# Optimization experiments

Hardware: AMD Instinct MI355X
Metric: run time of the kernel (lower is better)

## Reference

```python
import jax, jax.numpy as jnp
import numpy as np

ANISO = (0.096, 0.096, 0.096)
BIG = 1e10  # stands in for +inf feature distance
SMOOTH = 1e-05


def _minplus(f, axis, w):
    # exact 1D squared distance transform along `axis` via min-plus conv:
    # g[i] = min_j f[j] + (w*(i-j))^2 ; vectorized over all other dims.
    f = jnp.moveaxis(f, axis, -1)
    n = f.shape[-1]
    idx = jnp.arange(n, dtype=f.dtype)
    d2 = (w * (idx[:, None] - idx[None, :])) ** 2  # [j, i]
    g = jnp.min(f[..., :, None] + d2, axis=-2)
    return jnp.moveaxis(g, -1, axis)


def _edt_multilabel(labels, num_labels):
    # labels: [b, X, Y, Z] int, values in [1, num_labels]
    # Multi-label euclidean distance transform (edt.edt semantics on gt+1):
    # for each voxel, distance to nearest voxel carrying a DIFFERENT label,
    # scaled by ANISO. Computed as per-label squared EDT fields (separable
    # min-plus per axis, exact) combined by excluding the voxel's own label.
    fields = []
    for L in range(1, num_labels + 1):  # small fixed loop over classes
        f = jnp.where(labels == L, 0.0, BIG).astype(jnp.float32)
        for ax, w in zip((1, 2, 3), ANISO):
            f = _minplus(f, ax, w)
        fields.append(f)
    D = jnp.stack(fields, axis=0)  # [L, b, X, Y, Z] squared distances
    own = jnp.moveaxis(jax.nn.one_hot(labels - 1, num_labels, dtype=jnp.float32), -1, 0)
    d2 = jnp.min(jnp.where(own > 0, BIG, D), axis=0)  # nearest different label
    return jnp.sqrt(d2)


def setup_inputs() -> dict:
    key = jax.random.key(0)
    kx, ky = jax.random.split(key)
    x = jax.random.uniform(kx, (2, 3, 64, 64, 64), dtype=jnp.float32)  # softmax probs
    y = jax.random.randint(ky, (2, 1, 64, 64, 64), 0, 3)  # label map, classes 0..2
    return {"x": x, "y": y}


def reference(x, y):
    b, c = x.shape[:2]
    yi = y[:, 0]  # [b, X, Y, Z]
    # scatter_(1, gt, 1) -> one hot over channel dim
    y_onehot = jnp.moveaxis(jax.nn.one_hot(yi, c, dtype=x.dtype), -1, 1)  # [b,c,X,Y,Z]
    # dt = edt(gt + 1) + 1 ; all labels >=1 so every voxel is 'foreground'
    dt = (_edt_multilabel(yi + 1, c) + 1.0)[:, None]  # [b,1,X,Y,Z]
    fp = x * (1.0 - y_onehot) * dt
    fn = (1.0 - x) * y_onehot * dt
    # do_bg=False (non-batch-dice path): drop background channel
    fp = fp[:, 1:]
    fn = fn[:, 1:]
    return jnp.mean(fp) + jnp.mean(fn) + SMOOTH
```

## Files before the change

kernel.cpp:

```cpp
#include <hip/hip_runtime.h>
#include <math.h>

#define BIGV 10000000000.0f
#define WA   0.096f

__device__ __forceinline__ float seed_dist2(unsigned long long mask, int i) {
    const unsigned long long mr = mask >> i;
    const unsigned long long ml = mask << (63 - i);
    const int dr = mr ? __builtin_ctzll(mr) : 1000;
    const int dl = ml ? __builtin_clzll(ml) : 1000;
    const int d  = dr < dl ? dr : dl;
    const float t = WA * (float)d;
    return (d > 63) ? BIGV : t * t;
}

__global__ __launch_bounds__(256) void pass_xz_kernel(const int* __restrict__ lab,
                                                      float* __restrict__ D) {
    const int ys = blockIdx.x, b = blockIdx.y, zq = blockIdx.z;
    const int lane = threadIdx.x & 63;
    const int wv   = threadIdx.x >> 6;

    __shared__ float sm[3][64][64];

    const int* lp = lab + b * 262144 + ys * 64;
    for (int z = wv * 16, e = z + 16; z < e; ++z) {
        const int lv = lp[z * 4096 + lane];
        const unsigned long long mk0 = __ballot(lv == 0);
        const unsigned long long mk1 = __ballot(lv == 1);
        const unsigned long long mk2 = __ballot(lv == 2);
        sm[0][z][lane] = seed_dist2(mk0, lane);
        sm[1][z][lane] = seed_dist2(mk1, lane);
        sm[2][z][lane] = seed_dist2(mk2, lane);
    }
    __syncthreads();

    const int i0 = zq * 16 + wv * 4;
    float m0[4], m1[4], m2[4];
#pragma unroll
    for (int ii = 0; ii < 4; ++ii) m0[ii] = m1[ii] = m2[ii] = __builtin_inff();

    for (int j = 0; j < 64; ++j) {
        const float a0 = sm[0][j][lane];
        const float a1 = sm[1][j][lane];
        const float a2 = sm[2][j][lane];
        const float fb = (float)(i0 - j);
#pragma unroll
        for (int ii = 0; ii < 4; ++ii) {
            const float t = WA * (fb + (float)ii);
            m0[ii] = fminf(m0[ii], __builtin_fmaf(t, t, a0));
            m1[ii] = fminf(m1[ii], __builtin_fmaf(t, t, a1));
            m2[ii] = fminf(m2[ii], __builtin_fmaf(t, t, a2));
        }
    }

    float* Dp = D + b * 3 * 262144 + ys * 64;
#pragma unroll
    for (int ii = 0; ii < 4; ++ii) {
        const int zo = (i0 + ii) * 4096 + lane;
        Dp[zo]              = m0[ii];
        Dp[262144 + zo]     = m1[ii];
        Dp[2 * 262144 + zo] = m2[ii];
    }
}

__global__ __launch_bounds__(256) void pass_y_kernel(const float* __restrict__ x,
                                                     const int* __restrict__ lab,
                                                     const float* __restrict__ D,
                                                     float* __restrict__ out) {
    const int z = blockIdx.x, b = blockIdx.y, yq = blockIdx.z;
    const int lane = threadIdx.x & 63;
    const int wv   = threadIdx.x >> 6;

    __shared__ float sm[3][64][64];
    {
        const float4* Dp4 = (const float4*)(D + b * 3 * 262144 + z * 4096);
        float4* s4 = (float4*)&sm[0][0][0];
        for (int t = threadIdx.x; t < 1024; t += 256) {
            s4[t]        = Dp4[t];
            s4[1024 + t] = Dp4[65536 + t];
            s4[2048 + t] = Dp4[131072 + t];
        }
    }
    __syncthreads();

    const int i0 = yq * 16 + wv * 4;
    float m0[4], m1[4], m2[4];
#pragma unroll
    for (int ii = 0; ii < 4; ++ii) m0[ii] = m1[ii] = m2[ii] = __builtin_inff();

    for (int j = 0; j < 64; ++j) {
        const float a0 = sm[0][j][lane];
        const float a1 = sm[1][j][lane];
        const float a2 = sm[2][j][lane];
        const float fb = (float)(i0 - j);
#pragma unroll
        for (int ii = 0; ii < 4; ++ii) {
            const float t = WA * (fb + (float)ii);
            m0[ii] = fminf(m0[ii], __builtin_fmaf(t, t, a0));
            m1[ii] = fminf(m1[ii], __builtin_fmaf(t, t, a1));
            m2[ii] = fminf(m2[ii], __builtin_fmaf(t, t, a2));
        }
    }

    float part = 0.0f;
#pragma unroll
    for (int ii = 0; ii < 4; ++ii) {
        const int yy  = i0 + ii;
        const int off = z * 4096 + yy * 64 + lane;
        const int lv  = lab[b * 262144 + off];
        const float x1 = x[(b * 3 + 1) * 262144 + off];
        const float x2 = x[(b * 3 + 2) * 262144 + off];
        const float d0  = (lv == 0) ? BIGV : m0[ii];
        const float d1  = (lv == 1) ? BIGV : m1[ii];
        const float d2m = (lv == 2) ? BIGV : m2[ii];
        const float dt  = sqrtf(fminf(d0, fminf(d1, d2m))) + 1.0f;
        const float t1  = (lv == 1) ? (1.0f - x1) : x1;
        const float t2  = (lv == 2) ? (1.0f - x2) : x2;
        part += (t1 + t2) * dt;
    }

#pragma unroll
    for (int o = 32; o; o >>= 1) part += __shfl_down(part, o);
    if (lane == 0)
        atomicAdd(out, part * (1.0f / 1048576.0f));
    if (blockIdx.x == 0 && blockIdx.y == 0 && blockIdx.z == 0 && threadIdx.x == 0)
        atomicAdd(out, 1e-5f);
}

extern "C" void kernel_launch(void* const* d_in, const int* in_sizes, int n_in,
                              void* d_out, int out_size, void* d_ws, size_t ws_size,
                              hipStream_t stream) {
    const float* x = (const float*)d_in[0];
    const int*   y = (const int*)d_in[1];
    float* D   = (float*)d_ws;
    float* out = (float*)d_out;

    hipMemsetAsync(out, 0, sizeof(float), stream);
    pass_xz_kernel<<<dim3(64, 2, 4), 256, 0, stream>>>(y, D);
    pass_y_kernel<<<dim3(64, 2, 4), 256, 0, stream>>>(x, y, D, out);
}
```

Before: 103.0 us.

## Fuse both EDT passes into one cooperative kernel with grid sync

Merges the xz-pass and y-pass kernels into a single cooperative launch of 512 blocks separated by grid.sync(), and drops the memset. Replaces the global atomicAdd reduction with per-block partials that block 0 reduces after a second grid sync. The aim is to remove kernel-launch and memset overhead on this small workload. In exchange it pays for two grid-wide barriers and needs all 512 blocks to be co-resident.

```diff
diff --git a/kernel.cpp b/kernel.cpp
--- a/kernel.cpp
+++ b/kernel.cpp
@@ -1,5 +1,8 @@
 #include <hip/hip_runtime.h>
+#include <hip/hip_cooperative_groups.h>
 #include <math.h>
+
+namespace cg = cooperative_groups;
 
 #define BIGV 10000000000.0f
 #define WA   0.096f
@@ -14,65 +17,64 @@
     return (d > 63) ? BIGV : t * t;
 }
 
-__global__ __launch_bounds__(256) void pass_xz_kernel(const int* __restrict__ lab,
-                                                      float* __restrict__ D) {
-    const int ys = blockIdx.x, b = blockIdx.y, zq = blockIdx.z;
+__global__ __launch_bounds__(256) void fused_kernel(const float* __restrict__ x,
+                                                    const int* __restrict__ lab,
+                                                    float* __restrict__ D,
+                                                    float* __restrict__ partials,
+                                                    float* __restrict__ out) {
+    cg::grid_group grid = cg::this_grid();
+    const int bid  = blockIdx.x;
     const int lane = threadIdx.x & 63;
     const int wv   = threadIdx.x >> 6;
 
     __shared__ float sm[3][64][64];
 
-    const int* lp = lab + b * 262144 + ys * 64;
-    for (int z = wv * 16, e = z + 16; z < e; ++z) {
-        const int lv = lp[z * 4096 + lane];
-        const unsigned long long mk0 = __ballot(lv == 0);
-        const unsigned long long mk1 = __ballot(lv == 1);
-        const unsigned long long mk2 = __ballot(lv == 2);
-        sm[0][z][lane] = seed_dist2(mk0, lane);
-        sm[1][z][lane] = seed_dist2(mk1, lane);
-        sm[2][z][lane] = seed_dist2(mk2, lane);
-    }
-    __syncthreads();
+    {
+        const int ys = bid & 63, b = (bid >> 6) & 1, zq = bid >> 7;
 
-    const int i0 = zq * 16 + wv * 4;
-    float m0[4], m1[4], m2[4];
+        const int* lp = lab + b * 262144 + ys * 64;
+        for (int z = wv * 16, e = z + 16; z < e; ++z) {
+            const int lv = lp[z * 4096 + lane];
+            sm[0][z][lane] = seed_dist2(__ballot(lv == 0), lane);
+            sm[1][z][lane] = seed_dist2(__ballot(lv == 1), lane);
+            sm[2][z][lane] = seed_dist2(__ballot(lv == 2), lane);
+        }
+        __syncthreads();
+
+        const int i0 = zq * 16 + wv * 4;
+        float m0[4], m1[4], m2[4];
 #pragma unroll
-    for (int ii = 0; ii < 4; ++ii) m0[ii] = m1[ii] = m2[ii] = __builtin_inff();
+        for (int ii = 0; ii < 4; ++ii) m0[ii] = m1[ii] = m2[ii] = __builtin_inff();
 
-    for (int j = 0; j < 64; ++j) {
-        const float a0 = sm[0][j][lane];
-        const float a1 = sm[1][j][lane];
-        const float a2 = sm[2][j][lane];
-        const float fb = (float)(i0 - j);
+        for (int j = 0; j < 64; ++j) {
+            const float a0 = sm[0][j][lane];
+            const float a1 = sm[1][j][lane];
+            const float a2 = sm[2][j][lane];
+            const float fb = (float)(i0 - j);
+#pragma unroll
+            for (int ii = 0; ii < 4; ++ii) {
+                const float t = WA * (fb + (float)ii);
+                m0[ii] = fminf(m0[ii], __builtin_fmaf(t, t, a0));
+                m1[ii] = fminf(m1[ii], __builtin_fmaf(t, t, a1));
+                m2[ii] = fminf(m2[ii], __builtin_fmaf(t, t, a2));
+            }
+        }
+
+        float* Dp = D + b * 3 * 262144 + ys * 64;
 #pragma unroll
         for (int ii = 0; ii < 4; ++ii) {
-            const float t = WA * (fb + (float)ii);
-            m0[ii] = fminf(m0[ii], __builtin_fmaf(t, t, a0));
-            m1[ii] = fminf(m1[ii], __builtin_fmaf(t, t, a1));
-            m2[ii] = fminf(m2[ii], __builtin_fmaf(t, t, a2));
+            const int zo = (i0 + ii) * 4096 + lane;
+            Dp[zo]              = m0[ii];
+            Dp[262144 + zo]     = m1[ii];
+            Dp[2 * 262144 + zo] = m2[ii];
         }
     }
 
-    float* Dp = D + b * 3 * 262144 + ys * 64;
-#pragma unroll
-    for (int ii = 0; ii < 4; ++ii) {
-        const int zo = (i0 + ii) * 4096 + lane;
-        Dp[zo]              = m0[ii];
-        Dp[262144 + zo]     = m1[ii];
-        Dp[2 * 262144 + zo] = m2[ii];
-    }
-}
+    grid.sync();
 
-__global__ __launch_bounds__(256) void pass_y_kernel(const float* __restrict__ x,
-                                                     const int* __restrict__ lab,
-                                                     const float* __restrict__ D,
-                                                     float* __restrict__ out) {
-    const int z = blockIdx.x, b = blockIdx.y, yq = blockIdx.z;
-    const int lane = threadIdx.x & 63;
-    const int wv   = threadIdx.x >> 6;
+    {
+        const int z = bid & 63, b = (bid >> 6) & 1, yq = bid >> 7;
 
-    __shared__ float sm[3][64][64];
-    {
         const float4* Dp4 = (const float4*)(D + b * 3 * 262144 + z * 4096);
         float4* s4 = (float4*)&sm[0][0][0];
         for (int t = threadIdx.x; t < 1024; t += 256) {
@@ -80,51 +82,66 @@
             s4[1024 + t] = Dp4[65536 + t];
             s4[2048 + t] = Dp4[131072 + t];
         }
-    }
-    __syncthreads();
+        __syncthreads();
 
-    const int i0 = yq * 16 + wv * 4;
-    float m0[4], m1[4], m2[4];
+        const int i0 = yq * 16 + wv * 4;
+        float m0[4], m1[4], m2[4];
 #pragma unroll
-    for (int ii = 0; ii < 4; ++ii) m0[ii] = m1[ii] = m2[ii] = __builtin_inff();
+        for (int ii = 0; ii < 4; ++ii) m0[ii] = m1[ii] = m2[ii] = __builtin_inff();
 
-    for (int j = 0; j < 64; ++j) {
-        const float a0 = sm[0][j][lane];
-        const float a1 = sm[1][j][lane];
-        const float a2 = sm[2][j][lane];
-        const float fb = (float)(i0 - j);
+        for (int j = 0; j < 64; ++j) {
+            const float a0 = sm[0][j][lane];
+            const float a1 = sm[1][j][lane];
+            const float a2 = sm[2][j][lane];
+            const float fb = (float)(i0 - j);
+#pragma unroll
+            for (int ii = 0; ii < 4; ++ii) {
+                const float t = WA * (fb + (float)ii);
+                m0[ii] = fminf(m0[ii], __builtin_fmaf(t, t, a0));
+                m1[ii] = fminf(m1[ii], __builtin_fmaf(t, t, a1));
+                m2[ii] = fminf(m2[ii], __builtin_fmaf(t, t, a2));
+            }
+        }
+
+        float part = 0.0f;
 #pragma unroll
         for (int ii = 0; ii < 4; ++ii) {
-            const float t = WA * (fb + (float)ii);
-            m0[ii] = fminf(m0[ii], __builtin_fmaf(t, t, a0));
-            m1[ii] = fminf(m1[ii], __builtin_fmaf(t, t, a1));
-            m2[ii] = fminf(m2[ii], __builtin_fmaf(t, t, a2));
+            const int yy  = i0 + ii;
+            const int off = z * 4096 + yy * 64 + lane;
+            const int lv  = lab[b * 262144 + off];
+            const float x1 = x[(b * 3 + 1) * 262144 + off];
+            const float x2 = x[(b * 3 + 2) * 262144 + off];
+            const float d0  = (lv == 0) ? BIGV : m0[ii];
+            const float d1  = (lv == 1) ? BIGV : m1[ii];
+            const float d2m = (lv == 2) ? BIGV : m2[ii];
+            const float dt  = sqrtf(fminf(d0, fminf(d1, d2m))) + 1.0f;
+            const float t1  = (lv == 1) ? (1.0f - x1) : x1;
+            const float t2  = (lv == 2) ? (1.0f - x2) : x2;
+            part += (t1 + t2) * dt;
         }
+
+#pragma unroll
+        for (int o = 32; o; o >>= 1) part += __shfl_down(part, o);
+
+        __syncthreads();
+        if (lane == 0) sm[0][0][wv] = part;
+        __syncthreads();
+        if (threadIdx.x == 0)
+            partials[bid] = sm[0][0][0] + sm[0][0][1] + sm[0][0][2] + sm[0][0][3];
     }
 
-    float part = 0.0f;
+    grid.sync();
+
+    if (bid == 0) {
+        float v = partials[threadIdx.x] + partials[threadIdx.x + 256];
 #pragma unroll
-    for (int ii = 0; ii < 4; ++ii) {
-        const int yy  = i0 + ii;
-        const int off = z * 4096 + yy * 64 + lane;
-        const int lv  = lab[b * 262144 + off];
-        const float x1 = x[(b * 3 + 1) * 262144 + off];
-        const float x2 = x[(b * 3 + 2) * 262144 + off];
-        const float d0  = (lv == 0) ? BIGV : m0[ii];
-        const float d1  = (lv == 1) ? BIGV : m1[ii];
-        const float d2m = (lv == 2) ? BIGV : m2[ii];
-        const float dt  = sqrtf(fminf(d0, fminf(d1, d2m))) + 1.0f;
-        const float t1  = (lv == 1) ? (1.0f - x1) : x1;
-        const float t2  = (lv == 2) ? (1.0f - x2) : x2;
-        part += (t1 + t2) * dt;
+        for (int o = 32; o; o >>= 1) v += __shfl_down(v, o);
+        if (lane == 0) sm[0][0][8 + wv] = v;
+        __syncthreads();
+        if (threadIdx.x == 0)
+            out[0] = (sm[0][0][8] + sm[0][0][9] + sm[0][0][10] + sm[0][0][11])
+                         * (1.0f / 1048576.0f) + 1e-5f;
     }
-
-#pragma unroll
-    for (int o = 32; o; o >>= 1) part += __shfl_down(part, o);
-    if (lane == 0)
-        atomicAdd(out, part * (1.0f / 1048576.0f));
-    if (blockIdx.x == 0 && blockIdx.y == 0 && blockIdx.z == 0 && threadIdx.x == 0)
-        atomicAdd(out, 1e-5f);
 }
 
 extern "C" void kernel_launch(void* const* d_in, const int* in_sizes, int n_in,
@@ -132,10 +149,11 @@
                               hipStream_t stream) {
     const float* x = (const float*)d_in[0];
     const int*   y = (const int*)d_in[1];
-    float* D   = (float*)d_ws;
-    float* out = (float*)d_out;
+    float* D        = (float*)d_ws;
+    float* partials = D + 6 * 262144;
+    float* out      = (float*)d_out;
 
-    hipMemsetAsync(out, 0, sizeof(float), stream);
-    pass_xz_kernel<<<dim3(64, 2, 4), 256, 0, stream>>>(y, D);
-    pass_y_kernel<<<dim3(64, 2, 4), 256, 0, stream>>>(x, y, D, out);
+    void* args[] = {(void*)&x, (void*)&y, (void*)&D, (void*)&partials, (void*)&out};
+    hipLaunchCooperativeKernel((const void*)fused_kernel, dim3(512), dim3(256),
+                               args, 0, stream);
 }
```

Result: slower. 178.5 us (+73.2%).
